# Optimization experiments

Hardware: AMD Instinct MI355X
Metric: run time of the kernel (lower is better)

The kernel has to match this reference:

```python
import jax, jax.numpy as jnp
import numpy as np

B, T, H, K = 64, 512, 768, 11
START_ID, END_ID = 9, 10  # tag_to_ix['<CLS>'], tag_to_ix['<SEP>']
NEG = -10000.0


def setup_inputs() -> dict:
    key = jax.random.key(0)
    k1, k2, k3, k4 = jax.random.split(key, 4)
    embeds = jax.random.normal(k1, (B, T, H), dtype=jnp.float32)
    W_fc = jax.random.normal(k2, (K, H), dtype=jnp.float32) * 0.02
    b_fc = jax.random.normal(k3, (K,), dtype=jnp.float32) * 0.02
    transitions = jax.random.normal(k4, (K, K), dtype=jnp.float32)
    # __init__ masking: no transition out of anything into START row, none into END col
    transitions = transitions.at[START_ID, :].set(NEG)
    transitions = transitions.at[:, END_ID].set(NEG)
    return {"embeds": embeds, "W_fc": W_fc, "b_fc": b_fc, "transitions": transitions}


def reference(embeds, W_fc, b_fc, transitions):
    # fc projection: feats[b,t,k] (PLM_crf path: encoder output -> Linear)
    feats = jnp.einsum('bth,kh->btk', embeds, W_fc) + b_fc  # [B,T,K]
    Bv, Tv, Kv = feats.shape

    # Viterbi: log_delta init -10000 except start tag; NOTE the original never
    # adds feats[:, 0] (loop starts at t=1), so we faithfully skip it too.
    log_delta0 = jnp.full((Bv, Kv), NEG, dtype=feats.dtype).at[:, START_ID].set(0.0)

    def step(log_delta, feat_t):
        # transitions[i, j]: score of moving from prev tag j to tag i
        scores = transitions[None, :, :] + log_delta[:, None, :]  # [B,K,K]
        psi_t = jnp.argmax(scores, axis=-1)                       # [B,K] best prev tag
        log_delta_new = jnp.max(scores, axis=-1) + feat_t         # [B,K]
        return log_delta_new, psi_t

    feats_seq = jnp.swapaxes(feats[:, 1:], 0, 1)                  # [T-1,B,K]
    log_delta, psi = jax.lax.scan(step, log_delta0, feats_seq)    # psi: [T-1,B,K]

    score = jnp.max(log_delta, axis=-1)                           # [B]
    last_tag = jnp.argmax(log_delta, axis=-1)                     # [B]

    # Backtrack: path[t] = psi[t+1][path[t+1]] for t = T-2 .. 0
    def back(next_tag, psi_t):
        tag = jnp.take_along_axis(psi_t, next_tag[:, None], axis=-1)[:, 0]
        return tag, tag

    _, path_rest = jax.lax.scan(back, last_tag, psi, reverse=True)  # [T-1,B]
    path = jnp.concatenate([jnp.swapaxes(path_rest, 0, 1), last_tag[:, None]], axis=1)  # [B,T]
    return score, path
```

## Files before the change

### kernel.cpp

```cpp
#include <hip/hip_runtime.h>

#define BB 64
#define TT 512
#define HH 768
#define KK 11
#define START_ID 9
#define NEGV -10000.0f

template <int CTRL>
__device__ __forceinline__ float dpp_add(float x) {
    int yi = __builtin_amdgcn_update_dpp(0, __float_as_int(x), CTRL, 0xF, 0xF, false);
    return x + __int_as_float(yi);
}

__device__ __forceinline__ float wave_sum_to_lane63(float x) {
    x = dpp_add<0x111>(x);
    x = dpp_add<0x112>(x);
    x = dpp_add<0x114>(x);
    x = dpp_add<0x118>(x);
    x = dpp_add<0x142>(x);
    x = dpp_add<0x143>(x);
    return x;
}

__device__ __forceinline__ float rlane(float v, int l) {
    return __int_as_float(__builtin_amdgcn_readlane(__float_as_int(v), l));
}

__global__ __launch_bounds__(256) void fc_kernel(const float* __restrict__ embeds,
                                                 const float* __restrict__ W,
                                                 const float* __restrict__ bias,
                                                 float* __restrict__ feats) {
    const int lane = threadIdx.x & 63;
    const int wave_id = (blockIdx.x * blockDim.x + threadIdx.x) >> 6;
    const int nwaves = (gridDim.x * blockDim.x) >> 6;

    float4 wf[KK][3];
#pragma unroll
    for (int k = 0; k < KK; ++k) {
        wf[k][0] = *reinterpret_cast<const float4*>(W + k * HH + 0   + lane * 4);
        wf[k][1] = *reinterpret_cast<const float4*>(W + k * HH + 256 + lane * 4);
        wf[k][2] = *reinterpret_cast<const float4*>(W + k * HH + 512 + lane * 4);
    }
    float bk[KK];
#pragma unroll
    for (int k = 0; k < KK; ++k) bk[k] = bias[k];

    for (int row = wave_id; row < BB * TT; row += nwaves) {
        const float* e = embeds + (size_t)row * HH;
        float4 e0 = *reinterpret_cast<const float4*>(e + 0   + lane * 4);
        float4 e1 = *reinterpret_cast<const float4*>(e + 256 + lane * 4);
        float4 e2 = *reinterpret_cast<const float4*>(e + 512 + lane * 4);

        float acc[KK];
#pragma unroll
        for (int k = 0; k < KK; ++k) {
            float4 w0 = wf[k][0], w1 = wf[k][1], w2 = wf[k][2];
            acc[k] = e0.x * w0.x + e0.y * w0.y + e0.z * w0.z + e0.w * w0.w
                   + e1.x * w1.x + e1.y * w1.y + e1.z * w1.z + e1.w * w1.w
                   + e2.x * w2.x + e2.y * w2.y + e2.z * w2.z + e2.w * w2.w;
        }
#pragma unroll
        for (int k = 0; k < KK; ++k) acc[k] = wave_sum_to_lane63(acc[k]);

        if (lane == 63) {
#pragma unroll
            for (int k = 0; k < KK; ++k) feats[(size_t)row * KK + k] = acc[k] + bk[k];
        }
    }
}

__global__ __launch_bounds__(256) void viterbi_kernel(const float* __restrict__ feats,
                                                      const float* __restrict__ trans,
                                                      float* __restrict__ out) {
    __shared__ __align__(16) float feats_lds[TT * KK];
    __shared__ __align__(16) float dh[(TT - 1) * 12];
    __shared__ int psi_lds[(TT - 1) * KK];
    __shared__ float tr_lds[KK * KK];
    __shared__ int comp[15 * KK];
    __shared__ int bt[16];
    __shared__ int sh_last;

    const int tid = threadIdx.x;
    const int b = blockIdx.x;

    {
        const float4* src = reinterpret_cast<const float4*>(feats + (size_t)b * TT * KK);
        float4* dst = reinterpret_cast<float4*>(feats_lds);
        for (int i = tid; i < TT * KK / 4; i += 256) dst[i] = src[i];
        if (tid < KK * KK) tr_lds[tid] = trans[tid];
    }
    __syncthreads();

    if (tid < 64) {
        const int i = tid;
        const int ci = (i < KK) ? i : 0;
        float tr[KK];
#pragma unroll
        for (int j = 0; j < KK; ++j) tr[j] = (i < KK) ? tr_lds[i * KK + j] : NEGV;

        float delta = (i == START_ID) ? 0.0f : NEGV;
        float feat_cur = feats_lds[1 * KK + ci];

        for (int t = 1; t < TT; ++t) {
            if (i < KK) dh[(t - 1) * 12 + i] = delta;
            int nt = (t + 1 < TT) ? (t + 1) : 1;
            float feat_next = feats_lds[nt * KK + ci];

            float dj[KK];
#pragma unroll
            for (int j = 0; j < KK; ++j) dj[j] = rlane(delta, j);
            float s[KK];
#pragma unroll
            for (int j = 0; j < KK; ++j) s[j] = tr[j] + dj[j];
            float t0 = fmaxf(fmaxf(s[0], s[1]), s[2]);
            float t1 = fmaxf(fmaxf(s[3], s[4]), s[5]);
            float t2 = fmaxf(fmaxf(s[6], s[7]), s[8]);
            float t3 = fmaxf(s[9], s[10]);
            float best = fmaxf(fmaxf(fmaxf(t0, t1), t2), t3);
            delta = best + feat_cur;
            feat_cur = feat_next;
        }

        float dfin[KK];
#pragma unroll
        for (int j = 0; j < KK; ++j) dfin[j] = rlane(delta, j);
        float best = dfin[0];
        int last = 0;
#pragma unroll
        for (int j = 1; j < KK; ++j) {
            bool c = dfin[j] > best;
            best = c ? dfin[j] : best;
            last = c ? j : last;
        }
        if (tid == 0) {
            out[b] = best;
            out[BB + (size_t)b * TT + (TT - 1)] = (float)last;
            sh_last = last;
        }
    }
    __syncthreads();

    {
        const int i = tid & 15;
        const int sg = tid >> 4;
        if (i < KK) {
            float tri[KK];
#pragma unroll
            for (int j = 0; j < KK; ++j) tri[j] = tr_lds[i * KK + j];
            for (int s = sg; s < TT - 1; s += 16) {
                const float4* dr = reinterpret_cast<const float4*>(dh + s * 12);
                float4 a = dr[0], c4 = dr[1], d4 = dr[2];
                float sc[KK] = {tri[0] + a.x,  tri[1] + a.y,  tri[2] + a.z,  tri[3] + a.w,
                                tri[4] + c4.x, tri[5] + c4.y, tri[6] + c4.z, tri[7] + c4.w,
                                tri[8] + d4.x, tri[9] + d4.y, tri[10] + d4.z};
                float bv = sc[0];
                int bj = 0;
#pragma unroll
                for (int j = 1; j < KK; ++j) {
                    bool c = sc[j] > bv;
                    bv = c ? sc[j] : bv;
                    bj = c ? j : bj;
                }
                psi_lds[s * KK + i] = bj;
            }
        }
    }
    __syncthreads();

    {
        const int c = tid >> 4;
        const int i = tid & 15;
        if (c < 15 && i < KK) {
            int cur = i;
            for (int s = c * 32 + 31; s >= c * 32; --s) cur = psi_lds[s * KK + cur];
            comp[c * KK + i] = cur;
        } else if (c == 15 && i == 0) {
            int cur = sh_last;
            float* po = out + BB + (size_t)b * TT;
            for (int s = TT - 2; s >= 480; --s) {
                cur = psi_lds[s * KK + cur];
                po[s] = (float)cur;
            }
            bt[15] = cur;
        }
    }
    __syncthreads();

    if (tid == 0) {
        for (int c = 14; c >= 1; --c) bt[c] = comp[c * KK + bt[c + 1]];
    }
    __syncthreads();

    if (tid < 15) {
        const int c = tid;
        int cur = bt[c + 1];
        float* po = out + BB + (size_t)b * TT;
        for (int s = c * 32 + 31; s >= c * 32; --s) {
            cur = psi_lds[s * KK + cur];
            po[s] = (float)cur;
        }
    }
}

extern "C" void kernel_launch(void* const* d_in, const int* in_sizes, int n_in,
                              void* d_out, int out_size, void* d_ws, size_t ws_size,
                              hipStream_t stream) {
    const float* embeds = (const float*)d_in[0];
    const float* W_fc   = (const float*)d_in[1];
    const float* b_fc   = (const float*)d_in[2];
    const float* trans  = (const float*)d_in[3];
    float* out = (float*)d_out;
    float* feats = (float*)d_ws;

    fc_kernel<<<1024, 256, 0, stream>>>(embeds, W_fc, b_fc, feats);
    viterbi_kernel<<<BB, 256, 0, stream>>>(feats, trans, out);
}
```

Baseline: 208.8 us.

## Process two rows per wave with packed FMA and unroll Viterbi feature prefetch

The FC kernel now gives each wave a fixed block of 8 rows and handles two rows per iteration, reusing the register-resident weights across both. It uses float2 vector multiplies so the compiler can emit packed FMA instructions. The Viterbi forward loop is unrolled by four with features prefetched four steps ahead from LDS, taking the LDS read latency off the serial dependency chain. The LDS feature buffer is padded so the prefetch can read past the end safely. This assumes the grid covers exactly 8 rows per wave and drops the grid-stride loop.

```diff
diff --git a/kernel.cpp b/kernel.cpp
--- a/kernel.cpp
+++ b/kernel.cpp
@@ -6,6 +6,8 @@
 #define KK 11
 #define START_ID 9
 #define NEGV -10000.0f
+
+typedef float vf2 __attribute__((ext_vector_type(2)));
 
 template <int CTRL>
 __device__ __forceinline__ float dpp_add(float x) {
@@ -33,39 +35,54 @@
                                                  float* __restrict__ feats) {
     const int lane = threadIdx.x & 63;
     const int wave_id = (blockIdx.x * blockDim.x + threadIdx.x) >> 6;
-    const int nwaves = (gridDim.x * blockDim.x) >> 6;
 
     float4 wf[KK][3];
 #pragma unroll
-    for (int k = 0; k < KK; ++k) {
-        wf[k][0] = *reinterpret_cast<const float4*>(W + k * HH + 0   + lane * 4);
-        wf[k][1] = *reinterpret_cast<const float4*>(W + k * HH + 256 + lane * 4);
-        wf[k][2] = *reinterpret_cast<const float4*>(W + k * HH + 512 + lane * 4);
-    }
+    for (int k = 0; k < KK; ++k)
+#pragma unroll
+        for (int r = 0; r < 3; ++r)
+            wf[k][r] = *reinterpret_cast<const float4*>(W + k * HH + r * 256 + lane * 4);
+
     float bk[KK];
 #pragma unroll
     for (int k = 0; k < KK; ++k) bk[k] = bias[k];
 
-    for (int row = wave_id; row < BB * TT; row += nwaves) {
-        const float* e = embeds + (size_t)row * HH;
-        float4 e0 = *reinterpret_cast<const float4*>(e + 0   + lane * 4);
-        float4 e1 = *reinterpret_cast<const float4*>(e + 256 + lane * 4);
-        float4 e2 = *reinterpret_cast<const float4*>(e + 512 + lane * 4);
-
-        float acc[KK];
+    const int base = wave_id * 8;
+#pragma unroll 1
+    for (int rr = 0; rr < 8; rr += 2) {
+        const float* ea = embeds + (size_t)(base + rr) * HH;
+        const float* eb = ea + HH;
+        float4 a0 = *reinterpret_cast<const float4*>(ea + 0   + lane * 4);
+        float4 a1 = *reinterpret_cast<const float4*>(ea + 256 + lane * 4);
+        float4 a2 = *reinterpret_cast<const float4*>(ea + 512 + lane * 4);
+        float4 b0 = *reinterpret_cast<const float4*>(eb + 0   + lane * 4);
+        float4 b1 = *reinterpret_cast<const float4*>(eb + 256 + lane * 4);
+        float4 b2 = *reinterpret_cast<const float4*>(eb + 512 + lane * 4);
+
+        vf2 va[6] = {{a0.x, a0.y}, {a0.z, a0.w}, {a1.x, a1.y},
+                     {a1.z, a1.w}, {a2.x, a2.y}, {a2.z, a2.w}};
+        vf2 vb[6] = {{b0.x, b0.y}, {b0.z, b0.w}, {b1.x, b1.y},
+                     {b1.z, b1.w}, {b2.x, b2.y}, {b2.z, b2.w}};
+
+        float rA[KK], rB[KK];
 #pragma unroll
         for (int k = 0; k < KK; ++k) {
-            float4 w0 = wf[k][0], w1 = wf[k][1], w2 = wf[k][2];
-            acc[k] = e0.x * w0.x + e0.y * w0.y + e0.z * w0.z + e0.w * w0.w
-                   + e1.x * w1.x + e1.y * w1.y + e1.z * w1.z + e1.w * w1.w
-                   + e2.x * w2.x + e2.y * w2.y + e2.z * w2.z + e2.w * w2.w;
-        }
-#pragma unroll
-        for (int k = 0; k < KK; ++k) acc[k] = wave_sum_to_lane63(acc[k]);
-
+            vf2 wv[6] = {{wf[k][0].x, wf[k][0].y}, {wf[k][0].z, wf[k][0].w},
+                         {wf[k][1].x, wf[k][1].y}, {wf[k][1].z, wf[k][1].w},
+                         {wf[k][2].x, wf[k][2].y}, {wf[k][2].z, wf[k][2].w}};
+            vf2 sA = va[0] * wv[0];
+            vf2 sB = vb[0] * wv[0];
+#pragma unroll
+            for (int r = 1; r < 6; ++r) { sA += va[r] * wv[r]; sB += vb[r] * wv[r]; }
+            rA[k] = wave_sum_to_lane63(sA.x + sA.y);
+            rB[k] = wave_sum_to_lane63(sB.x + sB.y);
+        }
         if (lane == 63) {
-#pragma unroll
-            for (int k = 0; k < KK; ++k) feats[(size_t)row * KK + k] = acc[k] + bk[k];
+            float* oA = feats + (size_t)(base + rr) * KK;
+#pragma unroll
+            for (int k = 0; k < KK; ++k) oA[k] = rA[k] + bk[k];
+#pragma unroll
+            for (int k = 0; k < KK; ++k) oA[KK + k] = rB[k] + bk[k];
         }
     }
 }
@@ -73,7 +90,7 @@
 __global__ __launch_bounds__(256) void viterbi_kernel(const float* __restrict__ feats,
                                                       const float* __restrict__ trans,
                                                       float* __restrict__ out) {
-    __shared__ __align__(16) float feats_lds[TT * KK];
+    __shared__ __align__(16) float feats_lds[(TT + 4) * KK];
     __shared__ __align__(16) float dh[(TT - 1) * 12];
     __shared__ int psi_lds[(TT - 1) * KK];
     __shared__ float tr_lds[KK * KK];
@@ -100,13 +117,9 @@
         for (int j = 0; j < KK; ++j) tr[j] = (i < KK) ? tr_lds[i * KK + j] : NEGV;
 
         float delta = (i == START_ID) ? 0.0f : NEGV;
-        float feat_cur = feats_lds[1 * KK + ci];
-
-        for (int t = 1; t < TT; ++t) {
+
+        auto vstep = [&](int t, float fcur) {
             if (i < KK) dh[(t - 1) * 12 + i] = delta;
-            int nt = (t + 1 < TT) ? (t + 1) : 1;
-            float feat_next = feats_lds[nt * KK + ci];
-
             float dj[KK];
 #pragma unroll
             for (int j = 0; j < KK; ++j) dj[j] = rlane(delta, j);
@@ -118,9 +131,25 @@
             float t2 = fmaxf(fmaxf(s[6], s[7]), s[8]);
             float t3 = fmaxf(s[9], s[10]);
             float best = fmaxf(fmaxf(fmaxf(t0, t1), t2), t3);
-            delta = best + feat_cur;
-            feat_cur = feat_next;
-        }
+            delta = best + fcur;
+        };
+
+        float fr0 = feats_lds[1 * KK + ci];
+        float fr1 = feats_lds[2 * KK + ci];
+        float fr2 = feats_lds[3 * KK + ci];
+        float fr3 = feats_lds[4 * KK + ci];
+
+        int t = 1;
+#pragma unroll 1
+        for (; t <= TT - 4; t += 4) {
+            vstep(t,     fr0); fr0 = feats_lds[(t + 4) * KK + ci];
+            vstep(t + 1, fr1); fr1 = feats_lds[(t + 5) * KK + ci];
+            vstep(t + 2, fr2); fr2 = feats_lds[(t + 6) * KK + ci];
+            vstep(t + 3, fr3); fr3 = feats_lds[(t + 7) * KK + ci];
+        }
+        vstep(TT - 3, fr0);
+        vstep(TT - 2, fr1);
+        vstep(TT - 1, fr2);
 
         float dfin[KK];
 #pragma unroll
```

After: 202.9 us. 1.03x faster.
